# Performance work log

Hardware: AMD Instinct MI355X
Metric: run time of the kernel (lower is better)

## Reference

```python
import jax, jax.numpy as jnp
import numpy as np

EPS = 1e-5
N_HEADS = 8

def _layernorm(h, g, b):
    mu = jnp.mean(h, axis=-1, keepdims=True)
    var = jnp.mean((h - mu) ** 2, axis=-1, keepdims=True)
    return g * (h - mu) * jax.lax.rsqrt(var + EPS) + b

def _mlp_ln(x, W1, b1, W2, b2, g, beta):
    # Linear -> SiLU -> Linear -> LayerNorm (torch nn.Sequential processor)
    h = jax.nn.silu(x @ W1.T + b1)
    h = h @ W2.T + b2
    return _layernorm(h, g, beta)

def setup_inputs() -> dict:
    key = jax.random.key(0)
    ks = jax.random.split(key, 16)
    B, S, D = 4, 2048, 1024
    M, P, C = 128, 256, 512
    def lin(k, o, i):
        return (jax.random.normal(k, (o, i), jnp.float32) / np.sqrt(i)).astype(jnp.float32)
    inp = {}
    inp['x'] = jax.random.normal(ks[0], (B, S, D), jnp.float32)
    inp['scale_types'] = jax.random.randint(ks[1], (B, S), 0, 3)
    for name, dim, k1, k2 in [('mol', M, 2, 3), ('path', P, 4, 5), ('cell', C, 6, 7)]:
        inp[name + '_W1'] = lin(ks[k1], dim, D)
        inp[name + '_b1'] = jnp.zeros((dim,), jnp.float32)
        inp[name + '_W2'] = lin(ks[k2], dim, dim)
        inp[name + '_b2'] = jnp.zeros((dim,), jnp.float32)
        inp[name + '_g'] = jnp.ones((dim,), jnp.float32)
        inp[name + '_beta'] = jnp.zeros((dim,), jnp.float32)
    inp['int_W1'] = lin(ks[8], D, M + P + C)
    inp['int_b1'] = jnp.zeros((D,), jnp.float32)
    inp['int_W2'] = lin(ks[9], D, D)
    inp['int_b2'] = jnp.zeros((D,), jnp.float32)
    inp['int_g'] = jnp.ones((D,), jnp.float32)
    inp['int_beta'] = jnp.zeros((D,), jnp.float32)
    inp['attn_Wqkv'] = lin(ks[10], 3 * D, D)
    inp['attn_bqkv'] = jnp.zeros((3 * D,), jnp.float32)
    inp['attn_Wo'] = lin(ks[11], D, D)
    inp['attn_bo'] = jnp.zeros((D,), jnp.float32)
    inp['scale_w'] = jnp.ones((3,), jnp.float32) / 3.0
    return inp

def reference(x, scale_types,
              mol_W1, mol_b1, mol_W2, mol_b2, mol_g, mol_beta,
              path_W1, path_b1, path_W2, path_b2, path_g, path_beta,
              cell_W1, cell_b1, cell_W2, cell_b2, cell_g, cell_beta,
              int_W1, int_b1, int_W2, int_b2, int_g, int_beta,
              attn_Wqkv, attn_bqkv, attn_Wo, attn_bo, scale_w):
    B, S, D = x.shape
    # per-token routing: each token goes through exactly one expert; the
    # other two scale outputs are zeros (mask instead of Python loop).
    mol = _mlp_ln(x, mol_W1, mol_b1, mol_W2, mol_b2, mol_g, mol_beta) * (scale_types == 0)[..., None]
    path = _mlp_ln(x, path_W1, path_b1, path_W2, path_b2, path_g, path_beta) * (scale_types == 1)[..., None]
    cell = _mlp_ln(x, cell_W1, cell_b1, cell_W2, cell_b2, cell_g, cell_beta) * (scale_types == 2)[..., None]
    cat = jnp.concatenate([mol, path, cell], axis=-1)  # [B,S,M+P+C]
    integrated = _layernorm(jax.nn.silu(cat @ int_W1.T + int_b1) @ int_W2.T + int_b2, int_g, int_beta)
    # torch nn.MultiheadAttention (batch_first, self-attention)
    Dh = D // N_HEADS
    qkv = integrated @ attn_Wqkv.T + attn_bqkv  # [B,S,3D]
    q, k, v = jnp.split(qkv, 3, axis=-1)
    q = q.reshape(B, S, N_HEADS, Dh)
    k = k.reshape(B, S, N_HEADS, Dh)
    v = v.reshape(B, S, N_HEADS, Dh)
    scores = jnp.einsum('bqhd,bkhd->bhqk', q, k) / np.sqrt(Dh).astype(np.float32)
    attn = jax.nn.softmax(scores, axis=-1)
    o = jnp.einsum('bhqk,bkhd->bqhd', attn, v).reshape(B, S, D)
    attended = o @ attn_Wo.T + attn_bo
    w = jax.nn.softmax(scale_w, axis=0)
    final = integrated + w[0] * attended
    return (final, mol, path, cell)
```

## Files before the change

kernel.cpp:

```cpp
#include <hip/hip_runtime.h>
#include <cstdint>
#include <cstddef>

typedef unsigned short u16;
typedef unsigned int u32;
typedef short bf16x8 __attribute__((ext_vector_type(8)));
typedef float f32x4 __attribute__((ext_vector_type(4)));

__device__ __forceinline__ float bf2f(u16 u){
  union { u32 i; float f; } c; c.i = ((u32)u) << 16; return c.f;
}
__device__ __forceinline__ u16 f2bf(float f){
  union { float f; u32 i; } c; c.f = f;
  u32 r = c.i + 0x7FFFu + ((c.i >> 16) & 1u);
  return (u16)(r >> 16);
}
__device__ __forceinline__ void gload_lds16(const void* g, void* l){
  __builtin_amdgcn_global_load_lds(
      (const __attribute__((address_space(1))) u32*)g,
      (__attribute__((address_space(3))) u32*)l, 16, 0, 0);
}

struct ConvArgs {
  const float* src[11];
  u16* dst[11];
  u32 base[12];
};
__global__ __launch_bounds__(256)
void f32_to_bf16_multi(ConvArgs a){
  u32 i = blockIdx.x * 256 + threadIdx.x;
  if (i >= a.base[11]) return;
  int j = 0;
  #pragma unroll
  for (int k = 1; k < 11; ++k) j += (i >= a.base[k]);
  u32 li = i - a.base[j];
  const float4* s = (const float4*)a.src[j] + (size_t)li * 2;
  float4 va = s[0], vb = s[1];
  u16 o[8] = {f2bf(va.x),f2bf(va.y),f2bf(va.z),f2bf(va.w),
              f2bf(vb.x),f2bf(vb.y),f2bf(vb.z),f2bf(vb.w)};
  *(uint4*)(a.dst[j] + (size_t)li * 8) = *(const uint4*)o;
}

__global__ __launch_bounds__(256)
void concat3_f32(const float* __restrict__ a, const float* __restrict__ b,
                 const float* __restrict__ c, float* __restrict__ d){
  int i = blockIdx.x * 256 + threadIdx.x;
  if (i < 128) d[i] = a[i];
  else if (i < 384) d[i] = b[i - 128];
  else if (i < 896) d[i] = c[i - 384];
}

template<int EPI>
__global__ __launch_bounds__(256, 2)
void gemm_bt(const u16* __restrict__ A, const u16* __restrict__ W,
             const float* __restrict__ bias, void* __restrict__ Cv,
             int M, int N, int K, int lda, int ldc,
             const u16* __restrict__ I, const float* __restrict__ sw)
{
  __shared__ __align__(16) u16 As[128*64];
  __shared__ __align__(16) u16 Bs[128*64];
  const int tid  = threadIdx.x;
  const int lane = tid & 63;
  const int wave = tid >> 6;
  const int wr = wave >> 1, wc = wave & 1;
  const int m0 = blockIdx.y * 128, n0 = blockIdx.x * 128;

  f32x4 acc[4][4];
  #pragma unroll
  for (int r=0;r<4;++r)
    #pragma unroll
    for (int c=0;c<4;++c)
      #pragma unroll
      for (int e=0;e<4;++e) acc[r][c][e] = 0.f;

  int srow[4], soff[4];
  #pragma unroll
  for (int j=0;j<4;++j){
    int rr = (wave*4 + j)*8 + (lane>>3);
    srow[j] = rr;
    soff[j] = ((lane & 7) ^ (rr & 7)) * 8;
  }

  for (int k0 = 0; k0 < K; k0 += 64){
    #pragma unroll
    for (int j=0;j<4;++j){
      gload_lds16(A + (size_t)(m0 + srow[j])*lda + k0 + soff[j], As + (wave*4+j)*512);
      gload_lds16(W + (size_t)(n0 + srow[j])*K   + k0 + soff[j], Bs + (wave*4+j)*512);
    }
    __syncthreads();
    #pragma unroll
    for (int ks=0; ks<2; ++ks){
      bf16x8 af[4], bfr[4];
      #pragma unroll
      for (int r=0;r<4;++r){
        int row = wr*64 + r*16 + (lane&15);
        int cs  = (ks*4 + (lane>>4)) ^ (row & 7);
        af[r] = *(const bf16x8*)(As + row*64 + cs*8);
      }
      #pragma unroll
      for (int c=0;c<4;++c){
        int row = wc*64 + c*16 + (lane&15);
        int cs  = (ks*4 + (lane>>4)) ^ (row & 7);
        bfr[c] = *(const bf16x8*)(Bs + row*64 + cs*8);
      }
      #pragma unroll
      for (int r=0;r<4;++r)
        #pragma unroll
        for (int c=0;c<4;++c)
          acc[r][c] = __builtin_amdgcn_mfma_f32_16x16x32_bf16(af[r], bfr[c], acc[r][c], 0,0,0);
    }
    __syncthreads();
  }

  float w0 = 0.f;
  if (EPI == 2){
    float s0 = sw[0], s1 = sw[1], s2 = sw[2];
    float mx = fmaxf(s0, fmaxf(s1, s2));
    float e0 = __expf(s0-mx), e1 = __expf(s1-mx), e2 = __expf(s2-mx);
    w0 = e0 / (e0 + e1 + e2);
  }
  u16*   C16 = (u16*)Cv;
  float* C32 = (float*)Cv;
  #pragma unroll
  for (int c=0;c<4;++c){
    int col = n0 + wc*64 + c*16 + (lane&15);
    float bv = bias[col];
    #pragma unroll
    for (int r=0;r<4;++r){
      int rbase = m0 + wr*64 + r*16 + (lane>>4)*4;
      #pragma unroll
      for (int e=0;e<4;++e){
        int row = rbase + e;
        float v = acc[r][c][e] + bv;
        if (EPI == 1) v = v / (1.f + __expf(-v));
        if (EPI == 2){
          v = bf2f(I[(size_t)row*ldc + col]) + w0 * v;
          C32[(size_t)row*ldc + col] = v;
        } else {
          C16[(size_t)row*ldc + col] = f2bf(v);
        }
      }
    }
  }
}

template<int D, int MASK>
__global__ __launch_bounds__(256, 4)
void ln_k(u16* __restrict__ H, int ldh, const float* __restrict__ g,
          const float* __restrict__ beta, const int* __restrict__ st,
          int eid, void* __restrict__ outp)
{
  const int tid = threadIdx.x, lane = tid & 63, wave = tid >> 6;
  const int token = blockIdx.x * 4 + wave;
  constexpr int VPT = D / 64;
  float v[VPT];
  u16* row = H + (size_t)token * ldh + lane * VPT;
  #pragma unroll
  for (int i=0;i<VPT/2;++i){
    u32 u = ((const u32*)row)[i];
    v[2*i]   = bf2f((u16)(u & 0xFFFFu));
    v[2*i+1] = bf2f((u16)(u >> 16));
  }
  float s = 0.f;
  #pragma unroll
  for (int i=0;i<VPT;++i) s += v[i];
  #pragma unroll
  for (int off=1; off<64; off<<=1) s += __shfl_xor(s, off);
  float mu = s * (1.f / D);
  float q = 0.f;
  #pragma unroll
  for (int i=0;i<VPT;++i){ float d = v[i] - mu; q += d * d; }
  #pragma unroll
  for (int off=1; off<64; off<<=1) q += __shfl_xor(q, off);
  float rs = rsqrtf(q * (1.f / D) + 1e-5f);
  float msk = 1.f;
  if (MASK) msk = (st[token] == eid) ? 1.f : 0.f;
  #pragma unroll
  for (int i=0;i<VPT;++i){
    float gg = g[lane*VPT + i];
    float bb = beta[lane*VPT + i];
    float val = (gg * (v[i] - mu) * rs + bb) * msk;
    if (MASK){
      ((float*)outp)[(size_t)token * D + lane * VPT + i] = val;
      row[i] = f2bf(val);
    } else {
      ((u16*)outp)[(size_t)token * D + lane * VPT + i] = f2bf(val);
    }
  }
}

__global__ __launch_bounds__(256)
void transpose_v(const u16* __restrict__ qkv, u16* __restrict__ vt)
{
  __shared__ __align__(16) u16 T[64*72];
  const int tid = threadIdx.x;
  const int tt = blockIdx.x;
  const int dt = blockIdx.y;
  const int bh = blockIdx.z;
  const int b = bh >> 3, h = bh & 7;
  #pragma unroll
  for (int i=0;i<2;++i){
    int idx = tid + 256*i;
    int r = idx >> 3, c8 = idx & 7;
    const uint4* src = (const uint4*)(qkv + (size_t)(b*2048 + tt*64 + r)*3072
                                      + 2048 + h*128 + dt*64 + c8*8);
    *(uint4*)(T + r*72 + ((c8 ^ (r>>3)) & 7)*8) = *src;
  }
  __syncthreads();
  #pragma unroll
  for (int i=0;i<2;++i){
    int idx = tid + 256*i;
    int dr = idx >> 3, tc = idx & 7;
    u16 tmp[8];
    #pragma unroll
    for (int j=0;j<8;++j){
      int kap = tc*8 + j;
      int hp = kap >> 5, r2 = kap & 31;
      int srow = hp*32 + ((r2 & 1) ? 16 + (r2 >> 1) : (r2 >> 1));
      tmp[j] = T[srow*72 + (((dr>>3) ^ (srow>>3)) & 7)*8 + (dr & 7)];
    }
    *(uint4*)(vt + ((size_t)bh*128 + dt*64 + dr)*2048 + tt*64 + tc*8) = *(const uint4*)tmp;
  }
}

__global__ __launch_bounds__(256, 3)
void flash_attn(const u16* __restrict__ qkv, const u16* __restrict__ vt,
                u16* __restrict__ o)
{
  __shared__ __align__(16) u16 Ks[8192];
  __shared__ __align__(16) u16 Vs[8192];
  __shared__ __align__(16) u16 Ps[4*1152];
  const int tid = threadIdx.x, lane = tid & 63, wave = tid >> 6;
  const int b = blockIdx.z, h = blockIdx.y, q0 = blockIdx.x * 64;
  const float scale = 0.08838834764831845f;
  const float cl2   = 0.12751791892f;
  const float DEFER = 90.50966799187809f;

  bf16x8 qreg[4];
  {
    const u16* qrow = qkv + (size_t)(b*2048 + q0 + wave*16 + (lane&15))*3072
                      + h*128 + (lane>>4)*8;
    #pragma unroll
    for (int kk=0;kk<4;++kk) qreg[kk] = *(const bf16x8*)(qrow + kk*32);
  }
  asm volatile("s_waitcnt vmcnt(0)" ::: "memory");

  const u16* ksrc[4]; const u16* vsrc[4]; int cdst[4];
  #pragma unroll
  for (int i=0;i<4;++i){
    int cidx = (wave*4 + i)*64 + lane;
    int krow = cidx >> 4, kcs = cidx & 15;
    int kcsrc = (kcs & 8) | ((kcs & 7) ^ (krow & 7));
    ksrc[i] = qkv + (size_t)(b*2048 + krow)*3072 + h*128 + 1024 + kcsrc*8;
    int vd = cidx >> 3, vcs = cidx & 7;
    vsrc[i] = vt + ((size_t)(b*8 + h)*128 + vd)*2048 + (vcs ^ (vd & 7))*8;
    cdst[i] = cidx * 8;
  }

  auto stageK = [&](int kt){
    #pragma unroll
    for (int i=0;i<4;++i) gload_lds16(ksrc[i] + (size_t)kt*196608, Ks + cdst[i]);
  };
  auto stageV = [&](int kt){
    #pragma unroll
    for (int i=0;i<4;++i) gload_lds16(vsrc[i] + kt*64, Vs + cdst[i]);
  };

  f32x4 oacc[8];
  #pragma unroll
  for (int f=0;f<8;++f)
    #pragma unroll
    for (int e=0;e<4;++e) oacc[f][e] = 0.f;
  float m_run[4] = {-3e38f,-3e38f,-3e38f,-3e38f};
  float l_run[4] = {0.f,0.f,0.f,0.f};
  u16* PsW  = Ps + wave*1152;
  u32* PsW32 = (u32*)PsW;

  stageK(0);
  stageV(0);
  asm volatile("s_waitcnt vmcnt(4)" ::: "memory");
  __builtin_amdgcn_s_barrier();
  __builtin_amdgcn_sched_barrier(0);

  for (int kt=0; kt<32; ++kt){
    f32x4 s[4];
    #pragma unroll
    for (int cb=0;cb<4;++cb)
      #pragma unroll
      for (int e=0;e<4;++e) s[cb][e] = 0.f;
    __builtin_amdgcn_s_setprio(1);
    #pragma unroll
    for (int kk=0;kk<4;++kk){
      #pragma unroll
      for (int cb=0;cb<4;++cb){
        int row  = (lane&15) + 16*cb;
        int c    = kk*4 + (lane>>4);
        int slot = (c & 8) | ((c & 7) ^ (row & 7));
        bf16x8 bk = *(const bf16x8*)(Ks + row*128 + slot*8);
        s[cb] = __builtin_amdgcn_mfma_f32_16x16x32_bf16(qreg[kk], bk, s[cb], 0,0,0);
      }
    }
    __builtin_amdgcn_s_setprio(0);
    asm volatile("s_waitcnt lgkmcnt(0)" ::: "memory");
    __builtin_amdgcn_sched_barrier(0);
    __builtin_amdgcn_s_barrier();
    __builtin_amdgcn_sched_barrier(0);
    stageK((kt+1)&31);

    #pragma unroll
    for (int e=0;e<4;++e){
      float t0 = s[0][e], t1 = s[1][e], t2 = s[2][e], t3 = s[3][e];
      float lmx = fmaxf(fmaxf(t0,t1), fmaxf(t2,t3));
      if (__any(lmx > m_run[e] + DEFER)){
        float mx = lmx;
        #pragma unroll
        for (int off=1; off<16; off<<=1) mx = fmaxf(mx, __shfl_xor(mx, off));
        float mnew = fmaxf(m_run[e], mx);
        float a = exp2f((m_run[e] - mnew) * cl2);
        m_run[e] = mnew;
        l_run[e] *= a;
        #pragma unroll
        for (int f=0;f<8;++f) oacc[f][e] *= a;
      }
      float ms = m_run[e];
      float p0 = exp2f((t0 - ms)*cl2), p1 = exp2f((t1 - ms)*cl2);
      float p2 = exp2f((t2 - ms)*cl2), p3 = exp2f((t3 - ms)*cl2);
      l_run[e] += (p0 + p1) + (p2 + p3);
      u32 c01, c23;
      asm("v_cvt_pk_bf16_f32 %0, %1, %2" : "=v"(c01) : "v"(p0), "v"(p1));
      asm("v_cvt_pk_bf16_f32 %0, %1, %2" : "=v"(c23) : "v"(p2), "v"(p3));
      int prow = (lane>>4)*4 + e;
      PsW32[prow*36 +      (lane&15)] = c01;
      PsW32[prow*36 + 16 + (lane&15)] = c23;
    }

    asm volatile("s_waitcnt vmcnt(4)" ::: "memory");
    __builtin_amdgcn_sched_barrier(0);
    __builtin_amdgcn_s_barrier();
    __builtin_amdgcn_sched_barrier(0);

    __builtin_amdgcn_s_setprio(1);
    #pragma unroll
    for (int kk=0;kk<2;++kk){
      bf16x8 pa = *(const bf16x8*)(PsW + (lane&15)*72 + kk*32 + (lane>>4)*8);
      #pragma unroll
      for (int f=0;f<8;++f){
        int d = f*16 + (lane&15);
        int c = kk*4 + (lane>>4);
        bf16x8 vb = *(const bf16x8*)(Vs + d*64 + (c ^ (d & 7))*8);
        oacc[f] = __builtin_amdgcn_mfma_f32_16x16x32_bf16(pa, vb, oacc[f], 0,0,0);
      }
    }
    __builtin_amdgcn_s_setprio(0);
    asm volatile("s_waitcnt lgkmcnt(0) vmcnt(0)" ::: "memory");
    __builtin_amdgcn_sched_barrier(0);
    __builtin_amdgcn_s_barrier();
    __builtin_amdgcn_sched_barrier(0);
    if (kt + 1 < 32) stageV(kt+1);
  }

  #pragma unroll
  for (int e=0;e<4;++e){
    float l = l_run[e];
    #pragma unroll
    for (int off=1; off<16; off<<=1) l += __shfl_xor(l, off);
    l_run[e] = 1.f / l;
  }
  #pragma unroll
  for (int f=0;f<8;++f)
    #pragma unroll
    for (int e=0;e<4;++e){
      int row = q0 + wave*16 + (lane>>4)*4 + e;
      int col = h*128 + f*16 + (lane&15);
      o[(size_t)(b*2048 + row)*1024 + col] = f2bf(oacc[f][e] * l_run[e]);
    }
}

extern "C" void kernel_launch(void* const* d_in, const int* in_sizes, int n_in,
                              void* d_out, int out_size, void* d_ws, size_t ws_size,
                              hipStream_t stream)
{
  const float* x         = (const float*)d_in[0];
  const int*   stypes    = (const int*)d_in[1];
  const float* mol_W1    = (const float*)d_in[2];
  const float* mol_b1    = (const float*)d_in[3];
  const float* mol_W2    = (const float*)d_in[4];
  const float* mol_b2    = (const float*)d_in[5];
  const float* mol_g     = (const float*)d_in[6];
  const float* mol_beta  = (const float*)d_in[7];
  const float* path_W1   = (const float*)d_in[8];
  const float* path_b1   = (const float*)d_in[9];
  const float* path_W2   = (const float*)d_in[10];
  const float* path_b2   = (const float*)d_in[11];
  const float* path_g    = (const float*)d_in[12];
  const float* path_beta = (const float*)d_in[13];
  const float* cell_W1   = (const float*)d_in[14];
  const float* cell_b1   = (const float*)d_in[15];
  const float* cell_W2   = (const float*)d_in[16];
  const float* cell_b2   = (const float*)d_in[17];
  const float* cell_g    = (const float*)d_in[18];
  const float* cell_beta = (const float*)d_in[19];
  const float* int_W1    = (const float*)d_in[20];
  const float* int_b1    = (const float*)d_in[21];
  const float* int_W2    = (const float*)d_in[22];
  const float* int_b2    = (const float*)d_in[23];
  const float* int_g     = (const float*)d_in[24];
  const float* int_beta  = (const float*)d_in[25];
  const float* attn_Wqkv = (const float*)d_in[26];
  const float* attn_bqkv = (const float*)d_in[27];
  const float* attn_Wo   = (const float*)d_in[28];
  const float* attn_bo   = (const float*)d_in[29];
  const float* scale_w   = (const float*)d_in[30];

  float* out_final = (float*)d_out;
  float* out_mol   = out_final + 8388608;
  float* out_path  = out_mol   + 1048576;
  float* out_cell  = out_path  + 2097152;

  u16* ws    = (u16*)d_ws;
  u16* qkv   = ws;
  u16* integ = qkv   + 25165824;
  u16* S1    = integ + 8388608;
  u16* S2    = S1    + 8388608;
  u16* wb    = S2    + 8388608;
  u16* xb    = qkv;

  u16* w1f    = wb;
  u16* molW2b = w1f    + 917504;
  u16* pathW2b= molW2b + 16384;
  u16* cellW2b= pathW2b+ 65536;
  u16* intW1b = cellW2b+ 262144;
  u16* intW2b = intW1b + 917504;
  u16* qkvWb  = intW2b + 1048576;
  u16* woWb   = qkvWb  + 3145728;
  float* fbias= (float*)(woWb + 1048576);

  dim3 blk(256);
  const int M = 8192;

  ConvArgs ca;
  const float* srcs[11] = {x, mol_W1, path_W1, cell_W1, mol_W2, path_W2,
                           cell_W2, int_W1, int_W2, attn_Wqkv, attn_Wo};
  u16* dsts[11] = {xb, w1f, w1f + 131072, w1f + 393216, molW2b, pathW2b,
                   cellW2b, intW1b, intW2b, qkvWb, woWb};
  u32 n8s[11] = {1048576, 16384, 32768, 65536, 2048, 8192,
                 32768, 114688, 131072, 393216, 131072};
  u32 acc8 = 0;
  for (int i=0;i<11;++i){ ca.src[i]=srcs[i]; ca.dst[i]=dsts[i]; ca.base[i]=acc8; acc8+=n8s[i]; }
  ca.base[11] = acc8;
  f32_to_bf16_multi<<<(acc8 + 255)/256, blk, 0, stream>>>(ca);
  concat3_f32<<<4, blk, 0, stream>>>(mol_b1, path_b1, cell_b1, fbias);

  gemm_bt<1><<<dim3(7,64), blk, 0, stream>>>(xb, w1f, fbias, S1, M, 896, 1024, 1024, 896, nullptr, nullptr);
  gemm_bt<0><<<dim3(1,64), blk, 0, stream>>>(S1,       molW2b,  mol_b2,  S2,       M, 128, 128, 896, 896, nullptr, nullptr);
  gemm_bt<0><<<dim3(2,64), blk, 0, stream>>>(S1 + 128, pathW2b, path_b2, S2 + 128, M, 256, 256, 896, 896, nullptr, nullptr);
  gemm_bt<0><<<dim3(4,64), blk, 0, stream>>>(S1 + 384, cellW2b, cell_b2, S2 + 384, M, 512, 512, 896, 896, nullptr, nullptr);
  ln_k<128,1><<<2048, blk, 0, stream>>>(S2,       896, mol_g,  mol_beta,  stypes, 0, out_mol);
  ln_k<256,1><<<2048, blk, 0, stream>>>(S2 + 128, 896, path_g, path_beta, stypes, 1, out_path);
  ln_k<512,1><<<2048, blk, 0, stream>>>(S2 + 384, 896, cell_g, cell_beta, stypes, 2, out_cell);

  gemm_bt<1><<<dim3(8,64), blk, 0, stream>>>(S2, intW1b, int_b1, S1, M, 1024, 896,  896,  1024, nullptr, nullptr);
  gemm_bt<0><<<dim3(8,64), blk, 0, stream>>>(S1, intW2b, int_b2, S2, M, 1024, 1024, 1024, 1024, nullptr, nullptr);
  ln_k<1024,0><<<2048, blk, 0, stream>>>(S2, 1024, int_g, int_beta, nullptr, 0, integ);

  gemm_bt<0><<<dim3(24,64), blk, 0, stream>>>(integ, qkvWb, attn_bqkv, qkv, M, 3072, 1024, 1024, 3072, nullptr, nullptr);
  transpose_v<<<dim3(32,2,32), blk, 0, stream>>>(qkv, S2);
  flash_attn<<<dim3(32,8,4), blk, 0, stream>>>(qkv, S2, S1);

  gemm_bt<2><<<dim3(8,64), blk, 0, stream>>>(S1, woWb, attn_bo, out_final, M, 1024, 1024, 1024, 1024, integ, scale_w);
}
```

Before: 368.9 us.

## Double flash-attention query tile per block and merge expert GEMM/LN launches

```diff
diff --git a/kernel.cpp b/kernel.cpp
--- a/kernel.cpp
+++ b/kernel.cpp
@@ -51,11 +51,12 @@
 }
 
 template<int EPI>
-__global__ __launch_bounds__(256, 2)
-void gemm_bt(const u16* __restrict__ A, const u16* __restrict__ W,
-             const float* __restrict__ bias, void* __restrict__ Cv,
-             int M, int N, int K, int lda, int ldc,
-             const u16* __restrict__ I, const float* __restrict__ sw)
+__device__ __forceinline__ void gemm_body(
+    const u16* __restrict__ A, const u16* __restrict__ W,
+    const float* __restrict__ bias, void* __restrict__ Cv,
+    int N, int K, int lda, int ldc,
+    const u16* __restrict__ I, const float* __restrict__ sw,
+    int bx, int by)
 {
   __shared__ __align__(16) u16 As[128*64];
   __shared__ __align__(16) u16 Bs[128*64];
@@ -63,7 +64,7 @@
   const int lane = tid & 63;
   const int wave = tid >> 6;
   const int wr = wave >> 1, wc = wave & 1;
-  const int m0 = blockIdx.y * 128, n0 = blockIdx.x * 128;
+  const int m0 = by * 128, n0 = bx * 128;
 
   f32x4 acc[4][4];
   #pragma unroll
@@ -144,11 +145,39 @@
   }
 }
 
-template<int D, int MASK>
-__global__ __launch_bounds__(256, 4)
-void ln_k(u16* __restrict__ H, int ldh, const float* __restrict__ g,
-          const float* __restrict__ beta, const int* __restrict__ st,
-          int eid, void* __restrict__ outp)
+template<int EPI>
+__global__ __launch_bounds__(256, 2)
+void gemm_bt(const u16* __restrict__ A, const u16* __restrict__ W,
+             const float* __restrict__ bias, void* __restrict__ Cv,
+             int N, int K, int lda, int ldc,
+             const u16* __restrict__ I, const float* __restrict__ sw)
+{
+  gemm_body<EPI>(A, W, bias, Cv, N, K, lda, ldc, I, sw, blockIdx.x, blockIdx.y);
+}
+
+__global__ __launch_bounds__(256, 2)
+void gemm_w2group(const u16* __restrict__ S1, u16* __restrict__ S2,
+                  const u16* __restrict__ w0, const u16* __restrict__ w1,
+                  const u16* __restrict__ w2, const float* __restrict__ b0,
+                  const float* __restrict__ b1, const float* __restrict__ b2)
+{
+  int bx = blockIdx.x;
+  if (bx < 64){
+    gemm_body<0>(S1, w0, b0, S2, 128, 128, 896, 896, nullptr, nullptr, 0, bx);
+  } else if (bx < 192){
+    int l = bx - 64;
+    gemm_body<0>(S1+128, w1, b1, S2+128, 256, 256, 896, 896, nullptr, nullptr, l>>6, l&63);
+  } else {
+    int l = bx - 192;
+    gemm_body<0>(S1+384, w2, b2, S2+384, 512, 512, 896, 896, nullptr, nullptr, l>>6, l&63);
+  }
+}
+
+template<int D>
+__device__ __forceinline__ void ln_body_masked(
+    u16* __restrict__ H, int ldh, const float* __restrict__ g,
+    const float* __restrict__ beta, const int* __restrict__ st,
+    int eid, float* __restrict__ outp)
 {
   const int tid = threadIdx.x, lane = tid & 63, wave = tid >> 6;
   const int token = blockIdx.x * 4 + wave;
@@ -173,19 +202,62 @@
   #pragma unroll
   for (int off=1; off<64; off<<=1) q += __shfl_xor(q, off);
   float rs = rsqrtf(q * (1.f / D) + 1e-5f);
-  float msk = 1.f;
-  if (MASK) msk = (st[token] == eid) ? 1.f : 0.f;
+  float msk = (st[token] == eid) ? 1.f : 0.f;
   #pragma unroll
   for (int i=0;i<VPT;++i){
     float gg = g[lane*VPT + i];
     float bb = beta[lane*VPT + i];
     float val = (gg * (v[i] - mu) * rs + bb) * msk;
-    if (MASK){
-      ((float*)outp)[(size_t)token * D + lane * VPT + i] = val;
-      row[i] = f2bf(val);
-    } else {
-      ((u16*)outp)[(size_t)token * D + lane * VPT + i] = f2bf(val);
-    }
+    outp[(size_t)token * D + lane * VPT + i] = val;
+    row[i] = f2bf(val);
+  }
+}
+
+__global__ __launch_bounds__(256, 4)
+void ln_expert(u16* __restrict__ S2,
+               const float* __restrict__ g0, const float* __restrict__ be0,
+               const float* __restrict__ g1, const float* __restrict__ be1,
+               const float* __restrict__ g2, const float* __restrict__ be2,
+               const int* __restrict__ st,
+               float* __restrict__ o0, float* __restrict__ o1,
+               float* __restrict__ o2)
+{
+  if (blockIdx.y == 0)      ln_body_masked<128>(S2,     896, g0, be0, st, 0, o0);
+  else if (blockIdx.y == 1) ln_body_masked<256>(S2+128, 896, g1, be1, st, 1, o1);
+  else                      ln_body_masked<512>(S2+384, 896, g2, be2, st, 2, o2);
+}
+
+__global__ __launch_bounds__(256, 4)
+void ln_int(const u16* __restrict__ H, const float* __restrict__ g,
+            const float* __restrict__ beta, u16* __restrict__ outp)
+{
+  const int tid = threadIdx.x, lane = tid & 63, wave = tid >> 6;
+  const int token = blockIdx.x * 4 + wave;
+  constexpr int D = 1024, VPT = 16;
+  float v[VPT];
+  const u16* row = H + (size_t)token * D + lane * VPT;
+  #pragma unroll
+  for (int i=0;i<VPT/2;++i){
+    u32 u = ((const u32*)row)[i];
+    v[2*i]   = bf2f((u16)(u & 0xFFFFu));
+    v[2*i+1] = bf2f((u16)(u >> 16));
+  }
+  float s = 0.f;
+  #pragma unroll
+  for (int i=0;i<VPT;++i) s += v[i];
+  #pragma unroll
+  for (int off=1; off<64; off<<=1) s += __shfl_xor(s, off);
+  float mu = s * (1.f / D);
+  float q = 0.f;
+  #pragma unroll
+  for (int i=0;i<VPT;++i){ float d = v[i] - mu; q += d * d; }
+  #pragma unroll
+  for (int off=1; off<64; off<<=1) q += __shfl_xor(q, off);
+  float rs = rsqrtf(q * (1.f / D) + 1e-5f);
+  #pragma unroll
+  for (int i=0;i<VPT;++i){
+    float val = g[lane*VPT + i] * (v[i] - mu) * rs + beta[lane*VPT + i];
+    outp[(size_t)token * D + lane * VPT + i] = f2bf(val);
   }
 }
 
@@ -229,19 +301,19 @@
 {
   __shared__ __align__(16) u16 Ks[8192];
   __shared__ __align__(16) u16 Vs[8192];
-  __shared__ __align__(16) u16 Ps[4*1152];
+  __shared__ __align__(16) u16 Ps[4*2304];
   const int tid = threadIdx.x, lane = tid & 63, wave = tid >> 6;
-  const int b = blockIdx.z, h = blockIdx.y, q0 = blockIdx.x * 64;
-  const float scale = 0.08838834764831845f;
+  const int b = blockIdx.z, h = blockIdx.y, q0 = blockIdx.x * 128;
   const float cl2   = 0.12751791892f;
   const float DEFER = 90.50966799187809f;
 
-  bf16x8 qreg[4];
-  {
-    const u16* qrow = qkv + (size_t)(b*2048 + q0 + wave*16 + (lane&15))*3072
+  bf16x8 qreg[2][4];
+  #pragma unroll
+  for (int a=0;a<2;++a){
+    const u16* qrow = qkv + (size_t)(b*2048 + q0 + wave*32 + a*16 + (lane&15))*3072
                       + h*128 + (lane>>4)*8;
     #pragma unroll
-    for (int kk=0;kk<4;++kk) qreg[kk] = *(const bf16x8*)(qrow + kk*32);
+    for (int kk=0;kk<4;++kk) qreg[a][kk] = *(const bf16x8*)(qrow + kk*32);
   }
   asm volatile("s_waitcnt vmcnt(0)" ::: "memory");
 
@@ -266,14 +338,19 @@
     for (int i=0;i<4;++i) gload_lds16(vsrc[i] + kt*64, Vs + cdst[i]);
   };
 
-  f32x4 oacc[8];
-  #pragma unroll
-  for (int f=0;f<8;++f)
-    #pragma unroll
-    for (int e=0;e<4;++e) oacc[f][e] = 0.f;
-  float m_run[4] = {-3e38f,-3e38f,-3e38f,-3e38f};
-  float l_run[4] = {0.f,0.f,0.f,0.f};
-  u16* PsW  = Ps + wave*1152;
+  f32x4 oacc[2][8];
+  #pragma unroll
+  for (int a=0;a<2;++a)
+    #pragma unroll
+    for (int f=0;f<8;++f)
+      #pragma unroll
+      for (int e=0;e<4;++e) oacc[a][f][e] = 0.f;
+  float m_run[2][4], l_run[2][4];
+  #pragma unroll
+  for (int a=0;a<2;++a)
+    #pragma unroll
+    for (int e=0;e<4;++e){ m_run[a][e] = -3e38f; l_run[a][e] = 0.f; }
+  u16* PsW  = Ps + wave*2304;
   u32* PsW32 = (u32*)PsW;
 
   stageK(0);
@@ -283,11 +360,13 @@
   __builtin_amdgcn_sched_barrier(0);
 
   for (int kt=0; kt<32; ++kt){
-    f32x4 s[4];
-    #pragma unroll
-    for (int cb=0;cb<4;++cb)
-      #pragma unroll
-      for (int e=0;e<4;++e) s[cb][e] = 0.f;
+    f32x4 s[2][4];
+    #pragma unroll
+    for (int a=0;a<2;++a)
+      #pragma unroll
+      for (int cb=0;cb<4;++cb)
+        #pragma unroll
+        for (int e=0;e<4;++e) s[a][cb][e] = 0.f;
     __builtin_amdgcn_s_setprio(1);
     #pragma unroll
     for (int kk=0;kk<4;++kk){
@@ -297,7 +376,8 @@
         int c    = kk*4 + (lane>>4);
         int slot = (c & 8) | ((c & 7) ^ (row & 7));
         bf16x8 bk = *(const bf16x8*)(Ks + row*128 + slot*8);
-        s[cb] = __builtin_amdgcn_mfma_f32_16x16x32_bf16(qreg[kk], bk, s[cb], 0,0,0);
+        s[0][cb] = __builtin_amdgcn_mfma_f32_16x16x32_bf16(qreg[0][kk], bk, s[0][cb], 0,0,0);
+        s[1][cb] = __builtin_amdgcn_mfma_f32_16x16x32_bf16(qreg[1][kk], bk, s[1][cb], 0,0,0);
       }
     }
     __builtin_amdgcn_s_setprio(0);
@@ -308,30 +388,33 @@
     stageK((kt+1)&31);
 
     #pragma unroll
-    for (int e=0;e<4;++e){
-      float t0 = s[0][e], t1 = s[1][e], t2 = s[2][e], t3 = s[3][e];
-      float lmx = fmaxf(fmaxf(t0,t1), fmaxf(t2,t3));
-      if (__any(lmx > m_run[e] + DEFER)){
-        float mx = lmx;
-        #pragma unroll
-        for (int off=1; off<16; off<<=1) mx = fmaxf(mx, __shfl_xor(mx, off));
-        float mnew = fmaxf(m_run[e], mx);
-        float a = exp2f((m_run[e] - mnew) * cl2);
-        m_run[e] = mnew;
-        l_run[e] *= a;
-        #pragma unroll
-        for (int f=0;f<8;++f) oacc[f][e] *= a;
-      }
-      float ms = m_run[e];
-      float p0 = exp2f((t0 - ms)*cl2), p1 = exp2f((t1 - ms)*cl2);
-      float p2 = exp2f((t2 - ms)*cl2), p3 = exp2f((t3 - ms)*cl2);
-      l_run[e] += (p0 + p1) + (p2 + p3);
-      u32 c01, c23;
-      asm("v_cvt_pk_bf16_f32 %0, %1, %2" : "=v"(c01) : "v"(p0), "v"(p1));
-      asm("v_cvt_pk_bf16_f32 %0, %1, %2" : "=v"(c23) : "v"(p2), "v"(p3));
-      int prow = (lane>>4)*4 + e;
-      PsW32[prow*36 +      (lane&15)] = c01;
-      PsW32[prow*36 + 16 + (lane&15)] = c23;
+    for (int a=0;a<2;++a){
+      #pragma unroll
+      for (int e=0;e<4;++e){
+        float t0 = s[a][0][e], t1 = s[a][1][e], t2 = s[a][2][e], t3 = s[a][3][e];
+        float lmx = fmaxf(fmaxf(t0,t1), fmaxf(t2,t3));
+        if (__any(lmx > m_run[a][e] + DEFER)){
+          float mx = lmx;
+          #pragma unroll
+          for (int off=1; off<16; off<<=1) mx = fmaxf(mx, __shfl_xor(mx, off));
+          float mnew = fmaxf(m_run[a][e], mx);
+          float al = exp2f((m_run[a][e] - mnew) * cl2);
+          m_run[a][e] = mnew;
+          l_run[a][e] *= al;
+          #pragma unroll
+          for (int f=0;f<8;++f) oacc[a][f][e] *= al;
+        }
+        float ms = m_run[a][e];
+        float p0 = exp2f((t0 - ms)*cl2), p1 = exp2f((t1 - ms)*cl2);
+        float p2 = exp2f((t2 - ms)*cl2), p3 = exp2f((t3 - ms)*cl2);
+        l_run[a][e] += (p0 + p1) + (p2 + p3);
+        u32 c01, c23;
+        asm("v_cvt_pk_bf16_f32 %0, %1, %2" : "=v"(c01) : "v"(p0), "v"(p1));
+        asm("v_cvt_pk_bf16_f32 %0, %1, %2" : "=v"(c23) : "v"(p2), "v"(p3));
+        int prow = a*16 + (lane>>4)*4 + e;
+        PsW32[prow*36 +      (lane&15)] = c01;
+        PsW32[prow*36 + 16 + (lane&15)] = c23;
+      }
     }
 
     asm volatile("s_waitcnt vmcnt(4)" ::: "memory");
@@ -342,13 +425,15 @@
     __builtin_amdgcn_s_setprio(1);
     #pragma unroll
     for (int kk=0;kk<2;++kk){
-      bf16x8 pa = *(const bf16x8*)(PsW + (lane&15)*72 + kk*32 + (lane>>4)*8);
+      bf16x8 pa0 = *(const bf16x8*)(PsW + ((lane&15)     )*72 + kk*32 + (lane>>4)*8);
+      bf16x8 pa1 = *(const bf16x8*)(PsW + (16 + (lane&15))*72 + kk*32 + (lane>>4)*8);
       #pragma unroll
       for (int f=0;f<8;++f){
         int d = f*16 + (lane&15);
         int c = kk*4 + (lane>>4);
         bf16x8 vb = *(const bf16x8*)(Vs + d*64 + (c ^ (d & 7))*8);
-        oacc[f] = __builtin_amdgcn_mfma_f32_16x16x32_bf16(pa, vb, oacc[f], 0,0,0);
+        oacc[0][f] = __builtin_amdgcn_mfma_f32_16x16x32_bf16(pa0, vb, oacc[0][f], 0,0,0);
+        oacc[1][f] = __builtin_amdgcn_mfma_f32_16x16x32_bf16(pa1, vb, oacc[1][f], 0,0,0);
       }
     }
     __builtin_amdgcn_s_setprio(0);
@@ -360,20 +445,24 @@
   }
 
   #pragma unroll
-  for (int e=0;e<4;++e){
-    float l = l_run[e];
-    #pragma unroll
-    for (int off=1; off<16; off<<=1) l += __shfl_xor(l, off);
-    l_run[e] = 1.f / l;
-  }
-  #pragma unroll
-  for (int f=0;f<8;++f)
+  for (int a=0;a<2;++a)
     #pragma unroll
     for (int e=0;e<4;++e){
-      int row = q0 + wave*16 + (lane>>4)*4 + e;
-      int col = h*128 + f*16 + (lane&15);
-      o[(size_t)(b*2048 + row)*1024 + col] = f2bf(oacc[f][e] * l_run[e]);
-    }
+      float l = l_run[a][e];
+      #pragma unroll
+      for (int off=1; off<16; off<<=1) l += __shfl_xor(l, off);
+      l_run[a][e] = 1.f / l;
+    }
+  #pragma unroll
+  for (int a=0;a<2;++a)
+    #pragma unroll
+    for (int f=0;f<8;++f)
+      #pragma unroll
+      for (int e=0;e<4;++e){
+        int row = q0 + wave*32 + a*16 + (lane>>4)*4 + e;
+        int col = h*128 + f*16 + (lane&15);
+        o[(size_t)(b*2048 + row)*1024 + col] = f2bf(oacc[a][f][e] * l_run[a][e]);
+      }
 }
 
 extern "C" void kernel_launch(void* const* d_in, const int* in_sizes, int n_in,
@@ -436,7 +525,6 @@
   float* fbias= (float*)(woWb + 1048576);
 
   dim3 blk(256);
-  const int M = 8192;
 
   ConvArgs ca;
   const float* srcs[11] = {x, mol_W1, path_W1, cell_W1, mol_W2, path_W2,
@@ -451,21 +539,20 @@
   f32_to_bf16_multi<<<(acc8 + 255)/256, blk, 0, stream>>>(ca);
   concat3_f32<<<4, blk, 0, stream>>>(mol_b1, path_b1, cell_b1, fbias);
 
-  gemm_bt<1><<<dim3(7,64), blk, 0, stream>>>(xb, w1f, fbias, S1, M, 896, 1024, 1024, 896, nullptr, nullptr);
-  gemm_bt<0><<<dim3(1,64), blk, 0, stream>>>(S1,       molW2b,  mol_b2,  S2,       M, 128, 128, 896, 896, nullptr, nullptr);
-  gemm_bt<0><<<dim3(2,64), blk, 0, stream>>>(S1 + 128, pathW2b, path_b2, S2 + 128, M, 256, 256, 896, 896, nullptr, nullptr);
-  gemm_bt<0><<<dim3(4,64), blk, 0, stream>>>(S1 + 384, cellW2b, cell_b2, S2 + 384, M, 512, 512, 896, 896, nullptr, nullptr);
-  ln_k<128,1><<<2048, blk, 0, stream>>>(S2,       896, mol_g,  mol_beta,  stypes, 0, out_mol);
-  ln_k<256,1><<<2048, blk, 0, stream>>>(S2 + 128, 896, path_g, path_beta, stypes, 1, out_path);
-  ln_k<512,1><<<2048, blk, 0, stream>>>(S2 + 384, 896, cell_g, cell_beta, stypes, 2, out_cell);
-
-  gemm_bt<1><<<dim3(8,64), blk, 0, stream>>>(S2, intW1b, int_b1, S1, M, 1024, 896,  896,  1024, nullptr, nullptr);
-  gemm_bt<0><<<dim3(8,64), blk, 0, stream>>>(S1, intW2b, int_b2, S2, M, 1024, 1024, 1024, 1024, nullptr, nullptr);
-  ln_k<1024,0><<<2048, blk, 0, stream>>>(S2, 1024, int_g, int_beta, nullptr, 0, integ);
-
-  gemm_bt<0><<<dim3(24,64), blk, 0, stream>>>(integ, qkvWb, attn_bqkv, qkv, M, 3072, 1024, 1024, 3072, nullptr, nullptr);
+  gemm_bt<1><<<dim3(7,64), blk, 0, stream>>>(xb, w1f, fbias, S1, 896, 1024, 1024, 896, nullptr, nullptr);
+  gemm_w2group<<<448, blk, 0, stream>>>(S1, S2, molW2b, pathW2b, cellW2b,
+                                        mol_b2, path_b2, cell_b2);
+  ln_expert<<<dim3(2048,3), blk, 0, stream>>>(S2, mol_g, mol_beta, path_g,
+                                              path_beta, cell_g, cell_beta,
+                                              stypes, out_mol, out_path, out_cell);
+
+  gemm_bt<1><<<dim3(8,64), blk, 0, stream>>>(S2, intW1b, int_b1, S1, 1024, 896,  896,  1024, nullptr, nullptr);
+  gemm_bt<0><<<dim3(8,64), blk, 0, stream>>>(S1, intW2b, int_b2, S2, 1024, 1024, 1024, 1024, nullptr, nullptr);
+  ln_int<<<2048, blk, 0, stream>>>(S2, int_g, int_beta, integ);
+
+  gemm_bt<0><<<dim3(24,64), blk, 0, stream>>>(integ, qkvWb, attn_bqkv, qkv, 3072, 1024, 1024, 3072, nullptr, nullptr);
   transpose_v<<<dim3(32,2,32), blk, 0, stream>>>(qkv, S2);
-  flash_attn<<<dim3(32,8,4), blk, 0, stream>>>(qkv, S2, S1);
-
-  gemm_bt<2><<<dim3(8,64), blk, 0, stream>>>(S1, woWb, attn_bo, out_final, M, 1024, 1024, 1024, 1024, integ, scale_w);
-}
+  flash_attn<<<dim3(16,8,4), blk, 0, stream>>>(qkv, S2, S1);
+
+  gemm_bt<2><<<dim3(8,64), blk, 0, stream>>>(S1, woWb, attn_bo, out_final, 1024, 1024, 1024, 1024, integ, scale_w);
+}
```

New measurement: 404.6 us. 1.1x slower.
